# Kernel optimization log

Hardware: AMD Instinct MI355X
Metric: run time of the kernel (lower is better)

## Reference

```python
import jax, jax.numpy as jnp
import numpy as np

NUM_HEADS = 12
HEAD_DIM = 64
LOGIT_SCALE_MAX = 4.605170185988092  # log(1/0.01), open_clip default
EPS = 1e-12  # F.normalize eps


def setup_inputs() -> dict:
    key = jax.random.key(0)
    ks = jax.random.split(key, 8)
    N, L, C = 2, 2048, 768
    return {
        "x": jax.random.normal(ks[0], (N, L, C), dtype=jnp.float32),
        "in_proj_w": jax.random.normal(ks[1], (3 * C, C), dtype=jnp.float32) * 0.02,
        "in_proj_b": jax.random.normal(ks[2], (3 * C,), dtype=jnp.float32) * 0.02,
        "logit_scale": jax.random.normal(ks[3], (NUM_HEADS, 1, 1), dtype=jnp.float32),
        "learned_scale": jnp.ones((NUM_HEADS,), dtype=jnp.float32),
        "out_proj_w": jax.random.normal(ks[4], (C, C), dtype=jnp.float32) * 0.02,
        "out_proj_b": jax.random.normal(ks[5], (C,), dtype=jnp.float32) * 0.02,
        "attn_mask": jnp.zeros((L, L), dtype=jnp.float32),
    }


def _l2norm(t):
    # F.normalize(dim=-1): x / max(||x||, eps)
    n = jnp.linalg.norm(t, axis=-1, keepdims=True)
    return t / jnp.maximum(n, EPS)


def reference(x, in_proj_w, in_proj_b, logit_scale, learned_scale,
              out_proj_w, out_proj_b, attn_mask):
    N, L, C = x.shape
    H, D = NUM_HEADS, HEAD_DIM
    # packed QKV projection: [N, L, 3C]
    qkv = jnp.einsum("nlc,fc->nlf", x, in_proj_w) + in_proj_b
    q, k, v = jnp.split(qkv, 3, axis=-1)
    # [N, L, C] -> [N, H, L, D]
    to_heads = lambda t: t.reshape(N, L, H, D).transpose(0, 2, 1, 3)
    q, k, v = to_heads(q), to_heads(k), to_heads(v)
    # cosine attention with clamped exp logit scale per head
    attn = jnp.einsum("nhld,nhmd->nhlm", _l2norm(q), _l2norm(k))
    ls = jnp.exp(jnp.minimum(logit_scale, LOGIT_SCALE_MAX))  # [H,1,1]
    attn = attn * ls[None]  # broadcast over [N,H,L,L]
    attn = attn + attn_mask  # additive mask [L,L]
    attn = jax.nn.softmax(attn, axis=-1)
    out = jnp.einsum("nhlm,nhmd->nhld", attn, v)
    # learned per-head output scale
    out = out * learned_scale[None, :, None, None]
    # [N,H,L,D] -> [N,L,C]
    out = out.transpose(0, 2, 1, 3).reshape(N, L, C)
    out = jnp.einsum("nlc,fc->nlf", out, out_proj_w) + out_proj_b
    return out
```

## Files before the change

kernel.cpp:

```cpp
#include <hip/hip_runtime.h>
#include <math.h>

#define NB   2
#define SEQ  2048
#define CH   768
#define NH   12
#define HD   64
#define F3   2304
#define LSMAX 4.605170185988092f
#define LOG2E 1.4426950408889634f

typedef _Float16 f16;
typedef __attribute__((ext_vector_type(8))) _Float16 f16x8;
typedef __attribute__((ext_vector_type(4))) _Float16 f16x4;
typedef __attribute__((ext_vector_type(2))) _Float16 f16x2;
typedef __attribute__((ext_vector_type(4))) float f32x4;

typedef __attribute__((address_space(3))) void lds_void;
typedef __attribute__((address_space(1))) const void gbl_cvoid;

#define QSZ   3145728
#define OATT  (3 * QSZ)
#define XHOFF 12582912
#define W1OFF 15728640
#define W2OFF 17498112
#define FLAGO 18087936

#define KP   72
#define VP   136
#define PPIT 76
#define GP2  72

__global__ __launch_bounds__(256) void cvt_f16(const float* __restrict__ X,
                                               const float* __restrict__ W1,
                                               const float* __restrict__ W2,
                                               const float* __restrict__ M,
                                               f16* __restrict__ Xh,
                                               f16* __restrict__ W1h,
                                               f16* __restrict__ W2h,
                                               int* __restrict__ flag)
{
    int tid = blockIdx.x * 256 + threadIdx.x;
    if (blockIdx.y == 3) {
        if (tid < 1048576) {
            float4 v = ((const float4*)M)[tid];
            bool nz = (v.x != 0.f) || (v.y != 0.f) || (v.z != 0.f) || (v.w != 0.f);
            if (__any(nz) && (threadIdx.x & 63) == 0) atomicOr(flag, 1);
        }
        return;
    }
    const float* src; f16* dst; int n4;
    switch (blockIdx.y) {
        case 0:  src = X;  dst = Xh;  n4 = 786432;  break;
        case 1:  src = W1; dst = W1h; n4 = 442368;  break;
        default: src = W2; dst = W2h; n4 = 147456;  break;
    }
    if (tid < n4) {
        float4 v = ((const float4*)src)[tid];
        f16x4 o = {(f16)v.x, (f16)v.y, (f16)v.z, (f16)v.w};
        ((f16x4*)dst)[tid] = o;
    }
}

__global__ __launch_bounds__(256, 4) void qkv_gemm(const f16* __restrict__ Xh,
                                                   const f16* __restrict__ Wh,
                                                   const float* __restrict__ bias,
                                                   const float* __restrict__ logit_scale,
                                                   f16* __restrict__ qkv16)
{
    __shared__ f16 As[2][128 * 32];
    __shared__ f16 Bs[2][128 * 32];
    const int t    = threadIdx.x;
    const int w    = t >> 6;
    const int lane = t & 63;
    const int quad = lane >> 4;
    const int sub  = lane & 15;
    const int wm   = w & 1, wn = w >> 1;
    const int f0   = blockIdx.x * 128;
    const int m0   = blockIdx.y * 128;

    const int s0 = t, s1 = 256 + t;
    const int r0 = s0 >> 2, cb0 = ((s0 & 3) ^ (r0 & 3)) * 8;
    const int r1 = s1 >> 2, cb1 = ((s1 & 3) ^ (r1 & 3)) * 8;
    const f16* ga0 = Xh + (size_t)(m0 + r0) * CH + cb0;
    const f16* ga1 = Xh + (size_t)(m0 + r1) * CH + cb1;
    const f16* gb0 = Wh + (size_t)(f0 + r0) * CH + cb0;
    const f16* gb1 = Wh + (size_t)(f0 + r1) * CH + cb1;

    f32x4 acc[4][4];
#pragma unroll
    for (int i = 0; i < 4; ++i)
#pragma unroll
        for (int j = 0; j < 4; ++j) acc[i][j] = (f32x4){0.f, 0.f, 0.f, 0.f};

    const int pch = (quad ^ (sub & 3)) * 8;

    __builtin_amdgcn_global_load_lds((gbl_cvoid*)(ga0), (lds_void*)&As[0][s0 * 8], 16, 0, 0);
    __builtin_amdgcn_global_load_lds((gbl_cvoid*)(ga1), (lds_void*)&As[0][s1 * 8], 16, 0, 0);
    __builtin_amdgcn_global_load_lds((gbl_cvoid*)(gb0), (lds_void*)&Bs[0][s0 * 8], 16, 0, 0);
    __builtin_amdgcn_global_load_lds((gbl_cvoid*)(gb1), (lds_void*)&Bs[0][s1 * 8], 16, 0, 0);
    __syncthreads();

    for (int k0 = 0; k0 < CH; k0 += 32) {
        const int cur = (k0 >> 5) & 1, nxt = cur ^ 1;
        if (k0 + 32 < CH) {
            __builtin_amdgcn_global_load_lds((gbl_cvoid*)(ga0 + k0 + 32), (lds_void*)&As[nxt][s0 * 8], 16, 0, 0);
            __builtin_amdgcn_global_load_lds((gbl_cvoid*)(ga1 + k0 + 32), (lds_void*)&As[nxt][s1 * 8], 16, 0, 0);
            __builtin_amdgcn_global_load_lds((gbl_cvoid*)(gb0 + k0 + 32), (lds_void*)&Bs[nxt][s0 * 8], 16, 0, 0);
            __builtin_amdgcn_global_load_lds((gbl_cvoid*)(gb1 + k0 + 32), (lds_void*)&Bs[nxt][s1 * 8], 16, 0, 0);
        }
        f16x8 af[4], bf[4];
#pragma unroll
        for (int i = 0; i < 4; ++i) {
            af[i] = *(const f16x8*)&As[cur][(wm * 64 + i * 16 + sub) * 32 + pch];
            bf[i] = *(const f16x8*)&Bs[cur][(wn * 64 + i * 16 + sub) * 32 + pch];
        }
#pragma unroll
        for (int i = 0; i < 4; ++i)
#pragma unroll
            for (int j = 0; j < 4; ++j)
                acc[i][j] = __builtin_amdgcn_mfma_f32_16x16x32_f16(af[i], bf[j], acc[i][j], 0, 0, 0);
        __syncthreads();
    }

    const int t3 = f0 / CH;
    const int h  = ((f0 + wn * 64) % CH) >> 6;
    f16* dst = qkv16 + (size_t)t3 * QSZ;
    float lsv = (t3 == 0) ? __expf(fminf(logit_scale[h], LSMAX)) * LOG2E : 1.0f;
    float bb[4];
#pragma unroll
    for (int j = 0; j < 4; ++j) bb[j] = bias[f0 + wn * 64 + j * 16 + sub];
#pragma unroll
    for (int i = 0; i < 4; ++i) {
#pragma unroll
        for (int r = 0; r < 4; ++r) {
            int m = m0 + wm * 64 + i * 16 + quad * 4 + r;
            int n = m >> 11, l = m & 2047;
            float v[4];
#pragma unroll
            for (int j = 0; j < 4; ++j) v[j] = acc[i][j][r] + bb[j];
            float scale = 1.0f;
            if (t3 < 2) {
                float ss = v[0] * v[0] + v[1] * v[1] + v[2] * v[2] + v[3] * v[3];
#pragma unroll
                for (int mk = 1; mk < 16; mk <<= 1) ss += __shfl_xor(ss, mk, 64);
                scale = 1.0f / fmaxf(sqrtf(ss), 1e-12f);
                if (t3 == 0) scale *= lsv;
            }
            f16* drow = dst + (((size_t)n * NH + h) * SEQ + l) * HD;
#pragma unroll
            for (int j = 0; j < 4; ++j)
                drow[j * 16 + sub] = (f16)(v[j] * scale);
        }
    }
}

__global__ __launch_bounds__(256, 3) void attn(const f16* __restrict__ Qh,
                                               const f16* __restrict__ Kh,
                                               const f16* __restrict__ Vh,
                                               const float* __restrict__ M32,
                                               const float* __restrict__ lscale,
                                               const int* __restrict__ flag,
                                               f16* __restrict__ Og)
{
    __shared__ f16 Ks[128 * KP];
    __shared__ f16 Vt[64 * VP];
    __shared__ f16 QP[64 * PPIT];

    const int t    = threadIdx.x;
    const int w    = t >> 6;
    const int lane = t & 63;
    const int quad = lane >> 4;
    const int sub  = lane & 15;
    const int qb   = blockIdx.x * 64;
    const int h    = blockIdx.y, n = blockIdx.z;
    const bool has_mask = (*flag) != 0;

    const f16* Qg = Qh + ((size_t)(n * NH + h) * SEQ + qb) * HD;
    const f16* Kg = Kh + (size_t)(n * NH + h) * SEQ * HD;
    const f16* Vg = Vh + (size_t)(n * NH + h) * SEQ * HD;
    const float* Mg = M32 + (size_t)(qb + w * 16 + quad * 4) * SEQ;

#pragma unroll
    for (int rep = 0; rep < 2; ++rep) {
        int id = rep * 256 + t;
        int row = id >> 3, c8 = id & 7;
        f16x8 v = *(const f16x8*)&Qg[row * 64 + c8 * 8];
        *(f16x4*)&QP[row * PPIT + c8 * 8 + 0] = (f16x4){v[0], v[1], v[2], v[3]};
        *(f16x4*)&QP[row * PPIT + c8 * 8 + 4] = (f16x4){v[4], v[5], v[6], v[7]};
    }

    const int krow = t >> 1;
    const int kcb  = (t & 1) * 32;
    f16x8 kr0, kr1, kr2, kr3, vr0, vr1, vr2, vr3;
    {
        const f16* kp = Kg + krow * 64 + kcb;
        kr0 = *(const f16x8*)(kp + 0);
        kr1 = *(const f16x8*)(kp + 8);
        kr2 = *(const f16x8*)(kp + 16);
        kr3 = *(const f16x8*)(kp + 24);
        const f16* vp = Vg + (2 * lane) * 64 + w * 16;
        vr0 = *(const f16x8*)(vp + 0);
        vr1 = *(const f16x8*)(vp + 8);
        vr2 = *(const f16x8*)(vp + 64);
        vr3 = *(const f16x8*)(vp + 72);
    }

    __syncthreads();
    f16x8 qf0, qf1;
    {
        f16x4 l0 = *(const f16x4*)&QP[(w * 16 + sub) * PPIT + quad * 8];
        f16x4 l1 = *(const f16x4*)&QP[(w * 16 + sub) * PPIT + quad * 8 + 4];
        f16x4 l2 = *(const f16x4*)&QP[(w * 16 + sub) * PPIT + 32 + quad * 8];
        f16x4 l3 = *(const f16x4*)&QP[(w * 16 + sub) * PPIT + 32 + quad * 8 + 4];
        qf0 = (f16x8){l0[0], l0[1], l0[2], l0[3], l1[0], l1[1], l1[2], l1[3]};
        qf1 = (f16x8){l2[0], l2[1], l2[2], l2[3], l3[0], l3[1], l3[2], l3[3]};
    }

    {
        f16* kd = &Ks[krow * KP + kcb];
        *(f16x8*)(kd + 0)  = kr0;
        *(f16x8*)(kd + 8)  = kr1;
        *(f16x8*)(kd + 16) = kr2;
        *(f16x8*)(kd + 24) = kr3;
#pragma unroll
        for (int j = 0; j < 8; ++j) {
            *(f16x2*)&Vt[(w * 16 + j) * VP + 2 * lane]     = (f16x2){vr0[j], vr2[j]};
            *(f16x2*)&Vt[(w * 16 + 8 + j) * VP + 2 * lane] = (f16x2){vr1[j], vr3[j]};
        }
    }
    __syncthreads();

    const f16x8 ones = {(f16)1.f, (f16)1.f, (f16)1.f, (f16)1.f,
                        (f16)1.f, (f16)1.f, (f16)1.f, (f16)1.f};
    f32x4 o[4];
    f32x4 l_acc = (f32x4){0.f, 0.f, 0.f, 0.f};
    float m_run[4];
#pragma unroll
    for (int dt = 0; dt < 4; ++dt) o[dt] = (f32x4){0.f, 0.f, 0.f, 0.f};
#pragma unroll
    for (int r = 0; r < 4; ++r) m_run[r] = -1e30f;

    const int NITER = SEQ / 128;
    for (int c = 0; c < NITER; ++c) {
        const int c0 = c * 128;
        if (c + 1 < NITER) {
            const f16* kp = Kg + (c0 + 128 + krow) * 64 + kcb;
            kr0 = *(const f16x8*)(kp + 0);
            kr1 = *(const f16x8*)(kp + 8);
            kr2 = *(const f16x8*)(kp + 16);
            kr3 = *(const f16x8*)(kp + 24);
            const f16* vp = Vg + (c0 + 128 + 2 * lane) * 64 + w * 16;
            vr0 = *(const f16x8*)(vp + 0);
            vr1 = *(const f16x8*)(vp + 8);
            vr2 = *(const f16x8*)(vp + 64);
            vr3 = *(const f16x8*)(vp + 72);
        }

        f32x4 s[8];
#pragma unroll
        for (int ct = 0; ct < 8; ++ct) {
            f16x8 kf0 = *(const f16x8*)&Ks[(ct * 16 + sub) * KP + quad * 8];
            f16x8 kf1 = *(const f16x8*)&Ks[(ct * 16 + sub) * KP + 32 + quad * 8];
            f32x4 a = (f32x4){0.f, 0.f, 0.f, 0.f};
            a = __builtin_amdgcn_mfma_f32_16x16x32_f16(qf0, kf0, a, 0, 0, 0);
            a = __builtin_amdgcn_mfma_f32_16x16x32_f16(qf1, kf1, a, 0, 0, 0);
            s[ct] = a;
        }
        if (has_mask) {
#pragma unroll
            for (int ct = 0; ct < 8; ++ct)
#pragma unroll
                for (int r = 0; r < 4; ++r)
                    s[ct][r] += LOG2E * Mg[(size_t)r * SEQ + c0 + ct * 16 + sub];
        }
        float mnew[4];
#pragma unroll
        for (int r = 0; r < 4; ++r) {
            float a01 = fmaxf(s[0][r], s[1][r]), a23 = fmaxf(s[2][r], s[3][r]);
            float a45 = fmaxf(s[4][r], s[5][r]), a67 = fmaxf(s[6][r], s[7][r]);
            mnew[r] = fmaxf(fmaxf(fmaxf(a01, a23), fmaxf(a45, a67)), m_run[r]);
        }
        {
            union { f16x2 h; int i; } p0, p1, v0, v1;
            p0.h = (f16x2){(f16)mnew[0], (f16)mnew[1]};
            p1.h = (f16x2){(f16)mnew[2], (f16)mnew[3]};
#pragma unroll
            for (int mk = 1; mk < 16; mk <<= 1) {
                v0.i = __shfl_xor(p0.i, mk, 64);
                v1.i = __shfl_xor(p1.i, mk, 64);
                p0.h = __builtin_elementwise_max(p0.h, v0.h);
                p1.h = __builtin_elementwise_max(p1.h, v1.h);
            }
            mnew[0] = (float)p0.h[0]; mnew[1] = (float)p0.h[1];
            mnew[2] = (float)p1.h[0]; mnew[3] = (float)p1.h[1];
        }
        float alpha[4];
#pragma unroll
        for (int r = 0; r < 4; ++r) {
            alpha[r] = exp2f(m_run[r] - mnew[r]);
            m_run[r] = mnew[r];
        }
#pragma unroll
        for (int dt = 0; dt < 4; ++dt)
#pragma unroll
            for (int r = 0; r < 4; ++r) o[dt][r] *= alpha[r];
#pragma unroll
        for (int r = 0; r < 4; ++r) l_acc[r] *= alpha[r];

#pragma unroll
        for (int hf = 0; hf < 2; ++hf) {
#pragma unroll
            for (int ct = 0; ct < 4; ++ct)
#pragma unroll
                for (int r = 0; r < 4; ++r) {
                    float p = exp2f(s[hf * 4 + ct][r] - mnew[r]);
                    QP[(w * 16 + quad * 4 + r) * PPIT + ct * 16 + sub] = (f16)p;
                }
            f16x4 p00 = *(const f16x4*)&QP[(w * 16 + sub) * PPIT + quad * 8];
            f16x4 p01 = *(const f16x4*)&QP[(w * 16 + sub) * PPIT + quad * 8 + 4];
            f16x4 p10 = *(const f16x4*)&QP[(w * 16 + sub) * PPIT + 32 + quad * 8];
            f16x4 p11 = *(const f16x4*)&QP[(w * 16 + sub) * PPIT + 32 + quad * 8 + 4];
            f16x8 pf0 = {p00[0], p00[1], p00[2], p00[3], p01[0], p01[1], p01[2], p01[3]};
            f16x8 pf1 = {p10[0], p10[1], p10[2], p10[3], p11[0], p11[1], p11[2], p11[3]};
            l_acc = __builtin_amdgcn_mfma_f32_16x16x32_f16(pf0, ones, l_acc, 0, 0, 0);
            l_acc = __builtin_amdgcn_mfma_f32_16x16x32_f16(pf1, ones, l_acc, 0, 0, 0);
#pragma unroll
            for (int dt = 0; dt < 4; ++dt) {
                f16x8 vf0 = *(const f16x8*)&Vt[(dt * 16 + sub) * VP + hf * 64 + quad * 8];
                f16x8 vf1 = *(const f16x8*)&Vt[(dt * 16 + sub) * VP + hf * 64 + 32 + quad * 8];
                o[dt] = __builtin_amdgcn_mfma_f32_16x16x32_f16(pf0, vf0, o[dt], 0, 0, 0);
                o[dt] = __builtin_amdgcn_mfma_f32_16x16x32_f16(pf1, vf1, o[dt], 0, 0, 0);
            }
        }

        if (c + 1 < NITER) {
            __syncthreads();
            f16* kd = &Ks[krow * KP + kcb];
            *(f16x8*)(kd + 0)  = kr0;
            *(f16x8*)(kd + 8)  = kr1;
            *(f16x8*)(kd + 16) = kr2;
            *(f16x8*)(kd + 24) = kr3;
#pragma unroll
            for (int j = 0; j < 8; ++j) {
                *(f16x2*)&Vt[(w * 16 + j) * VP + 2 * lane]     = (f16x2){vr0[j], vr2[j]};
                *(f16x2*)&Vt[(w * 16 + 8 + j) * VP + 2 * lane] = (f16x2){vr1[j], vr3[j]};
            }
            __syncthreads();
        }
    }
    float lsc = lscale[h];
#pragma unroll
    for (int r = 0; r < 4; ++r) {
        float inv = lsc / l_acc[r];
        int q = qb + w * 16 + quad * 4 + r;
#pragma unroll
        for (int dt = 0; dt < 4; ++dt)
            Og[((size_t)n * SEQ + q) * CH + h * 64 + dt * 16 + sub] =
                (f16)(o[dt][r] * inv);
    }
}

__global__ __launch_bounds__(256, 4) void out_gemm(const f16* __restrict__ A,
                                                   const f16* __restrict__ Wh,
                                                   const float* __restrict__ bias,
                                                   float* __restrict__ out)
{
    __shared__ f16 As[64 * GP2];
    __shared__ f16 Bs[64 * GP2];
    const int t    = threadIdx.x;
    const int w    = t >> 6;
    const int lane = t & 63;
    const int quad = lane >> 4;
    const int sub  = lane & 15;
    const int f0   = blockIdx.x * 64;
    const int m0   = blockIdx.y * 64;
    const int srow = t >> 2;
    const int sk   = (t & 3) * 16;

    const f16* ag = A + (size_t)(m0 + srow) * CH + sk;
    const f16* bg = Wh + (size_t)(f0 + srow) * CH + sk;
    f16x8 a0 = *(const f16x8*)(ag);
    f16x8 a1 = *(const f16x8*)(ag + 8);
    f16x8 b0 = *(const f16x8*)(bg);
    f16x8 b1 = *(const f16x8*)(bg + 8);

    f32x4 acc[4];
#pragma unroll
    for (int i = 0; i < 4; ++i) acc[i] = (f32x4){0.f, 0.f, 0.f, 0.f};

    for (int k0 = 0; k0 < CH; k0 += 64) {
        __syncthreads();
        *(f16x8*)&As[srow * GP2 + sk + 0] = a0;
        *(f16x8*)&As[srow * GP2 + sk + 8] = a1;
        *(f16x8*)&Bs[srow * GP2 + sk + 0] = b0;
        *(f16x8*)&Bs[srow * GP2 + sk + 8] = b1;
        __syncthreads();
        if (k0 + 64 < CH) {
            a0 = *(const f16x8*)(ag + k0 + 64);
            a1 = *(const f16x8*)(ag + k0 + 72);
            b0 = *(const f16x8*)(bg + k0 + 64);
            b1 = *(const f16x8*)(bg + k0 + 72);
        }
#pragma unroll
        for (int kk = 0; kk < 64; kk += 32) {
            f16x8 bf = *(const f16x8*)&Bs[(w * 16 + sub) * GP2 + kk + quad * 8];
#pragma unroll
            for (int i = 0; i < 4; ++i) {
                f16x8 af = *(const f16x8*)&As[(i * 16 + sub) * GP2 + kk + quad * 8];
                acc[i] = __builtin_amdgcn_mfma_f32_16x16x32_f16(af, bf, acc[i], 0, 0, 0);
            }
        }
    }
    float bb = bias[f0 + w * 16 + sub];
#pragma unroll
    for (int i = 0; i < 4; ++i)
#pragma unroll
        for (int r = 0; r < 4; ++r) {
            int m = m0 + i * 16 + quad * 4 + r;
            out[(size_t)m * CH + f0 + w * 16 + sub] = acc[i][r] + bb;
        }
}

extern "C" void kernel_launch(void* const* d_in, const int* in_sizes, int n_in,
                              void* d_out, int out_size, void* d_ws, size_t ws_size,
                              hipStream_t stream) {
    const float* x    = (const float*)d_in[0];
    const float* w1   = (const float*)d_in[1];
    const float* b1   = (const float*)d_in[2];
    const float* ls   = (const float*)d_in[3];
    const float* lrn  = (const float*)d_in[4];
    const float* w2   = (const float*)d_in[5];
    const float* b2   = (const float*)d_in[6];
    const float* msk  = (const float*)d_in[7];
    f16*   ws16 = (f16*)d_ws;
    int*   flag = (int*)(ws16 + FLAGO);
    float* out  = (float*)d_out;

    (void)hipMemsetAsync(flag, 0, 4, stream);
    hipLaunchKernelGGL(cvt_f16, dim3(4096, 4), dim3(256), 0, stream,
                       x, w1, w2, msk,
                       ws16 + XHOFF, ws16 + W1OFF, ws16 + W2OFF, flag);
    hipLaunchKernelGGL(qkv_gemm, dim3(F3 / 128, (NB * SEQ) / 128), dim3(256), 0, stream,
                       ws16 + XHOFF, ws16 + W1OFF, b1, ls, ws16);
    hipLaunchKernelGGL(attn, dim3(SEQ / 64, NH, NB), dim3(256), 0, stream,
                       ws16, ws16 + QSZ, ws16 + 2 * QSZ, msk, lrn, flag,
                       ws16 + OATT);
    hipLaunchKernelGGL(out_gemm, dim3(CH / 64, (NB * SEQ) / 64), dim3(256), 0, stream,
                       ws16 + OATT, ws16 + W2OFF, b2, out);
}
```

Before: 209.5 us.

## Rewrite attention with 32x32 MFMA, transposed V, and split-KV within block

The QKV GEMM epilogue now writes V transposed ([N,H,D,L]) so the attention kernel can load V fragments straight from global memory without an LDS transpose. The attention kernel drops LDS staging of K/V entirely. It computes S^T with 32x32x16 MFMAs so each lane owns one query row's probabilities in registers, which removes the LDS round trip for P and the cross-lane max shuffles. Each block splits the key range between two wave pairs and merges the partial softmax states through LDS at the end. The cost is that K/V tiles are no longer shared through LDS, so global and cache traffic per wave rises.

```diff
diff --git a/kernel.cpp b/kernel.cpp
--- a/kernel.cpp
+++ b/kernel.cpp
@@ -15,6 +15,7 @@
 typedef __attribute__((ext_vector_type(4))) _Float16 f16x4;
 typedef __attribute__((ext_vector_type(2))) _Float16 f16x2;
 typedef __attribute__((ext_vector_type(4))) float f32x4;
+typedef __attribute__((ext_vector_type(16))) float f32x16;
 
 typedef __attribute__((address_space(3))) void lds_void;
 typedef __attribute__((address_space(1))) const void gbl_cvoid;
@@ -26,9 +27,6 @@
 #define W2OFF 17498112
 #define FLAGO 18087936
 
-#define KP   72
-#define VP   136
-#define PPIT 76
 #define GP2  72
 
 __global__ __launch_bounds__(256) void cvt_f16(const float* __restrict__ X,
@@ -125,11 +123,30 @@
 
     const int t3 = f0 / CH;
     const int h  = ((f0 + wn * 64) % CH) >> 6;
+    float bb[4];
+#pragma unroll
+    for (int j = 0; j < 4; ++j) bb[j] = bias[f0 + wn * 64 + j * 16 + sub];
+
+    if (t3 == 2) {
+        f16* vdst = qkv16 + (size_t)2 * QSZ;
+#pragma unroll
+        for (int i = 0; i < 4; ++i) {
+            int mb = m0 + wm * 64 + i * 16 + quad * 4;
+            int nn = mb >> 11, l0 = mb & 2047;
+            f16* vrow = vdst + ((size_t)(nn * NH + h) * HD) * SEQ + l0;
+#pragma unroll
+            for (int j = 0; j < 4; ++j) {
+                f16x4 vv;
+#pragma unroll
+                for (int r = 0; r < 4; ++r) vv[r] = (f16)(acc[i][j][r] + bb[j]);
+                *(f16x4*)(vrow + (size_t)(j * 16 + sub) * SEQ) = vv;
+            }
+        }
+        return;
+    }
+
     f16* dst = qkv16 + (size_t)t3 * QSZ;
     float lsv = (t3 == 0) ? __expf(fminf(logit_scale[h], LSMAX)) * LOG2E : 1.0f;
-    float bb[4];
-#pragma unroll
-    for (int j = 0; j < 4; ++j) bb[j] = bias[f0 + wn * 64 + j * 16 + sub];
 #pragma unroll
     for (int i = 0; i < 4; ++i) {
 #pragma unroll
@@ -139,14 +156,11 @@
             float v[4];
 #pragma unroll
             for (int j = 0; j < 4; ++j) v[j] = acc[i][j][r] + bb[j];
-            float scale = 1.0f;
-            if (t3 < 2) {
-                float ss = v[0] * v[0] + v[1] * v[1] + v[2] * v[2] + v[3] * v[3];
-#pragma unroll
-                for (int mk = 1; mk < 16; mk <<= 1) ss += __shfl_xor(ss, mk, 64);
-                scale = 1.0f / fmaxf(sqrtf(ss), 1e-12f);
-                if (t3 == 0) scale *= lsv;
-            }
+            float ss = v[0] * v[0] + v[1] * v[1] + v[2] * v[2] + v[3] * v[3];
+#pragma unroll
+            for (int mk = 1; mk < 16; mk <<= 1) ss += __shfl_xor(ss, mk, 64);
+            float scale = 1.0f / fmaxf(sqrtf(ss), 1e-12f);
+            if (t3 == 0) scale *= lsv;
             f16* drow = dst + (((size_t)n * NH + h) * SEQ + l) * HD;
 #pragma unroll
             for (int j = 0; j < 4; ++j)
@@ -157,207 +171,156 @@
 
 __global__ __launch_bounds__(256, 3) void attn(const f16* __restrict__ Qh,
                                                const f16* __restrict__ Kh,
-                                               const f16* __restrict__ Vh,
+                                               const f16* __restrict__ Vt,
                                                const float* __restrict__ M32,
                                                const float* __restrict__ lscale,
                                                const int* __restrict__ flag,
                                                f16* __restrict__ Og)
 {
-    __shared__ f16 Ks[128 * KP];
-    __shared__ f16 Vt[64 * VP];
-    __shared__ f16 QP[64 * PPIT];
+    __shared__ float OS[2][32][68];
+    __shared__ float MS[2][32];
+    __shared__ float LS[2][32];
 
     const int t    = threadIdx.x;
     const int w    = t >> 6;
     const int lane = t & 63;
-    const int quad = lane >> 4;
-    const int sub  = lane & 15;
+    const int g    = w >> 1;
+    const int s    = w & 1;
+    const int r32  = lane & 31;
+    const int h2   = lane >> 5;
     const int qb   = blockIdx.x * 64;
-    const int h    = blockIdx.y, n = blockIdx.z;
+    const int hh   = blockIdx.y, n = blockIdx.z;
     const bool has_mask = (*flag) != 0;
 
-    const f16* Qg = Qh + ((size_t)(n * NH + h) * SEQ + qb) * HD;
-    const f16* Kg = Kh + (size_t)(n * NH + h) * SEQ * HD;
-    const f16* Vg = Vh + (size_t)(n * NH + h) * SEQ * HD;
-    const float* Mg = M32 + (size_t)(qb + w * 16 + quad * 4) * SEQ;
-
-#pragma unroll
-    for (int rep = 0; rep < 2; ++rep) {
-        int id = rep * 256 + t;
-        int row = id >> 3, c8 = id & 7;
-        f16x8 v = *(const f16x8*)&Qg[row * 64 + c8 * 8];
-        *(f16x4*)&QP[row * PPIT + c8 * 8 + 0] = (f16x4){v[0], v[1], v[2], v[3]};
-        *(f16x4*)&QP[row * PPIT + c8 * 8 + 4] = (f16x4){v[4], v[5], v[6], v[7]};
-    }
-
-    const int krow = t >> 1;
-    const int kcb  = (t & 1) * 32;
-    f16x8 kr0, kr1, kr2, kr3, vr0, vr1, vr2, vr3;
-    {
-        const f16* kp = Kg + krow * 64 + kcb;
-        kr0 = *(const f16x8*)(kp + 0);
-        kr1 = *(const f16x8*)(kp + 8);
-        kr2 = *(const f16x8*)(kp + 16);
-        kr3 = *(const f16x8*)(kp + 24);
-        const f16* vp = Vg + (2 * lane) * 64 + w * 16;
-        vr0 = *(const f16x8*)(vp + 0);
-        vr1 = *(const f16x8*)(vp + 8);
-        vr2 = *(const f16x8*)(vp + 64);
-        vr3 = *(const f16x8*)(vp + 72);
-    }
-
+    const int q = qb + g * 32 + r32;
+    const f16* Qg  = Qh + ((size_t)(n * NH + hh) * SEQ + q) * HD + 8 * h2;
+    const f16* Kl  = Kh + ((size_t)(n * NH + hh) * SEQ + s * 1024 + r32) * HD + 8 * h2;
+    const f16* Vb0 = Vt + ((size_t)(n * NH + hh) * HD + r32) * SEQ + s * 1024 + 4 * h2;
+    const f16* Vb1 = Vb0 + (size_t)32 * SEQ;
+    const float* Mg = M32 + (size_t)q * SEQ + s * 1024;
+
+    f16x8 qf0 = *(const f16x8*)(Qg + 0);
+    f16x8 qf1 = *(const f16x8*)(Qg + 16);
+    f16x8 qf2 = *(const f16x8*)(Qg + 32);
+    f16x8 qf3 = *(const f16x8*)(Qg + 48);
+
+    f16x8 kf0 = *(const f16x8*)(Kl + 0);
+    f16x8 kf1 = *(const f16x8*)(Kl + 16);
+    f16x8 kf2 = *(const f16x8*)(Kl + 32);
+    f16x8 kf3 = *(const f16x8*)(Kl + 48);
+
+    f32x16 o0 = {}, o1 = {};
+    float m_run = -1e30f, l_acc = 0.f;
+    const f16x2 one2 = {(f16)1.f, (f16)1.f};
+
+#pragma unroll 1
+    for (int c = 0; c < 32; ++c) {
+        const int k0 = c * 32;
+        f32x16 sA = {};
+        sA = __builtin_amdgcn_mfma_f32_32x32x16_f16(kf0, qf0, sA, 0, 0, 0);
+        sA = __builtin_amdgcn_mfma_f32_32x32x16_f16(kf1, qf1, sA, 0, 0, 0);
+        sA = __builtin_amdgcn_mfma_f32_32x32x16_f16(kf2, qf2, sA, 0, 0, 0);
+        sA = __builtin_amdgcn_mfma_f32_32x32x16_f16(kf3, qf3, sA, 0, 0, 0);
+        if (c + 1 < 32) {
+            const f16* kp = Kl + (size_t)(k0 + 32) * HD;
+            kf0 = *(const f16x8*)(kp + 0);
+            kf1 = *(const f16x8*)(kp + 16);
+            kf2 = *(const f16x8*)(kp + 32);
+            kf3 = *(const f16x8*)(kp + 48);
+        }
+        union V8 { f16x4 h[2]; f16x8 v; };
+        V8 va, vb, vc, vd;
+        va.h[0] = *(const f16x4*)(Vb0 + k0 + 0);
+        va.h[1] = *(const f16x4*)(Vb0 + k0 + 8);
+        vb.h[0] = *(const f16x4*)(Vb0 + k0 + 16);
+        vb.h[1] = *(const f16x4*)(Vb0 + k0 + 24);
+        vc.h[0] = *(const f16x4*)(Vb1 + k0 + 0);
+        vc.h[1] = *(const f16x4*)(Vb1 + k0 + 8);
+        vd.h[0] = *(const f16x4*)(Vb1 + k0 + 16);
+        vd.h[1] = *(const f16x4*)(Vb1 + k0 + 24);
+
+        if (has_mask) {
+#pragma unroll
+            for (int rr = 0; rr < 16; ++rr) {
+                int kk = k0 + (rr & 3) + 8 * (rr >> 2) + 4 * h2;
+                sA[rr] += LOG2E * Mg[kk];
+            }
+        }
+        float mloc = sA[0];
+#pragma unroll
+        for (int rr = 1; rr < 16; ++rr) mloc = fmaxf(mloc, sA[rr]);
+        float mfull = fmaxf(mloc, __shfl_xor(mloc, 32, 64));
+        float mnew = fmaxf(m_run, mfull);
+        float al = exp2f(m_run - mnew);
+        m_run = mnew;
+        l_acc *= al;
+#pragma unroll
+        for (int rr = 0; rr < 16; ++rr) { o0[rr] *= al; o1[rr] *= al; }
+
+        float p[16];
+#pragma unroll
+        for (int rr = 0; rr < 16; ++rr) p[rr] = exp2f(sA[rr] - m_run);
+        union U8 { int i[4]; f16x8 v; };
+#define PK(a, b) ({ f16x2 _t = {(f16)(a), (f16)(b)}; __builtin_bit_cast(int, _t); })
+        U8 u0, u1;
+        u0.i[0] = PK(p[0], p[1]);   u0.i[1] = PK(p[2], p[3]);
+        u0.i[2] = PK(p[4], p[5]);   u0.i[3] = PK(p[6], p[7]);
+        u1.i[0] = PK(p[8], p[9]);   u1.i[1] = PK(p[10], p[11]);
+        u1.i[2] = PK(p[12], p[13]); u1.i[3] = PK(p[14], p[15]);
+#undef PK
+        f16x8 pf0 = u0.v, pf1 = u1.v;
+
+        l_acc = __builtin_amdgcn_fdot2(__builtin_bit_cast(f16x2, u0.i[0]), one2, l_acc, false);
+        l_acc = __builtin_amdgcn_fdot2(__builtin_bit_cast(f16x2, u0.i[1]), one2, l_acc, false);
+        l_acc = __builtin_amdgcn_fdot2(__builtin_bit_cast(f16x2, u0.i[2]), one2, l_acc, false);
+        l_acc = __builtin_amdgcn_fdot2(__builtin_bit_cast(f16x2, u0.i[3]), one2, l_acc, false);
+        l_acc = __builtin_amdgcn_fdot2(__builtin_bit_cast(f16x2, u1.i[0]), one2, l_acc, false);
+        l_acc = __builtin_amdgcn_fdot2(__builtin_bit_cast(f16x2, u1.i[1]), one2, l_acc, false);
+        l_acc = __builtin_amdgcn_fdot2(__builtin_bit_cast(f16x2, u1.i[2]), one2, l_acc, false);
+        l_acc = __builtin_amdgcn_fdot2(__builtin_bit_cast(f16x2, u1.i[3]), one2, l_acc, false);
+
+        o0 = __builtin_amdgcn_mfma_f32_32x32x16_f16(va.v, pf0, o0, 0, 0, 0);
+        o0 = __builtin_amdgcn_mfma_f32_32x32x16_f16(vb.v, pf1, o0, 0, 0, 0);
+        o1 = __builtin_amdgcn_mfma_f32_32x32x16_f16(vc.v, pf0, o1, 0, 0, 0);
+        o1 = __builtin_amdgcn_mfma_f32_32x32x16_f16(vd.v, pf1, o1, 0, 0, 0);
+    }
+
+    float l_full = l_acc + __shfl_xor(l_acc, 32, 64);
+
+    if (s == 1) {
+        if (h2 == 0) { MS[g][r32] = m_run; LS[g][r32] = l_full; }
+#pragma unroll
+        for (int rq = 0; rq < 4; ++rq) {
+            int d0 = 8 * rq + 4 * h2;
+            *(f32x4*)&OS[g][r32][d0] =
+                (f32x4){o0[rq * 4 + 0], o0[rq * 4 + 1], o0[rq * 4 + 2], o0[rq * 4 + 3]};
+            *(f32x4*)&OS[g][r32][d0 + 32] =
+                (f32x4){o1[rq * 4 + 0], o1[rq * 4 + 1], o1[rq * 4 + 2], o1[rq * 4 + 3]};
+        }
+    }
     __syncthreads();
-    f16x8 qf0, qf1;
-    {
-        f16x4 l0 = *(const f16x4*)&QP[(w * 16 + sub) * PPIT + quad * 8];
-        f16x4 l1 = *(const f16x4*)&QP[(w * 16 + sub) * PPIT + quad * 8 + 4];
-        f16x4 l2 = *(const f16x4*)&QP[(w * 16 + sub) * PPIT + 32 + quad * 8];
-        f16x4 l3 = *(const f16x4*)&QP[(w * 16 + sub) * PPIT + 32 + quad * 8 + 4];
-        qf0 = (f16x8){l0[0], l0[1], l0[2], l0[3], l1[0], l1[1], l1[2], l1[3]};
-        qf1 = (f16x8){l2[0], l2[1], l2[2], l2[3], l3[0], l3[1], l3[2], l3[3]};
-    }
-
-    {
-        f16* kd = &Ks[krow * KP + kcb];
-        *(f16x8*)(kd + 0)  = kr0;
-        *(f16x8*)(kd + 8)  = kr1;
-        *(f16x8*)(kd + 16) = kr2;
-        *(f16x8*)(kd + 24) = kr3;
-#pragma unroll
-        for (int j = 0; j < 8; ++j) {
-            *(f16x2*)&Vt[(w * 16 + j) * VP + 2 * lane]     = (f16x2){vr0[j], vr2[j]};
-            *(f16x2*)&Vt[(w * 16 + 8 + j) * VP + 2 * lane] = (f16x2){vr1[j], vr3[j]};
-        }
-    }
-    __syncthreads();
-
-    const f16x8 ones = {(f16)1.f, (f16)1.f, (f16)1.f, (f16)1.f,
-                        (f16)1.f, (f16)1.f, (f16)1.f, (f16)1.f};
-    f32x4 o[4];
-    f32x4 l_acc = (f32x4){0.f, 0.f, 0.f, 0.f};
-    float m_run[4];
-#pragma unroll
-    for (int dt = 0; dt < 4; ++dt) o[dt] = (f32x4){0.f, 0.f, 0.f, 0.f};
-#pragma unroll
-    for (int r = 0; r < 4; ++r) m_run[r] = -1e30f;
-
-    const int NITER = SEQ / 128;
-    for (int c = 0; c < NITER; ++c) {
-        const int c0 = c * 128;
-        if (c + 1 < NITER) {
-            const f16* kp = Kg + (c0 + 128 + krow) * 64 + kcb;
-            kr0 = *(const f16x8*)(kp + 0);
-            kr1 = *(const f16x8*)(kp + 8);
-            kr2 = *(const f16x8*)(kp + 16);
-            kr3 = *(const f16x8*)(kp + 24);
-            const f16* vp = Vg + (c0 + 128 + 2 * lane) * 64 + w * 16;
-            vr0 = *(const f16x8*)(vp + 0);
-            vr1 = *(const f16x8*)(vp + 8);
-            vr2 = *(const f16x8*)(vp + 64);
-            vr3 = *(const f16x8*)(vp + 72);
-        }
-
-        f32x4 s[8];
-#pragma unroll
-        for (int ct = 0; ct < 8; ++ct) {
-            f16x8 kf0 = *(const f16x8*)&Ks[(ct * 16 + sub) * KP + quad * 8];
-            f16x8 kf1 = *(const f16x8*)&Ks[(ct * 16 + sub) * KP + 32 + quad * 8];
-            f32x4 a = (f32x4){0.f, 0.f, 0.f, 0.f};
-            a = __builtin_amdgcn_mfma_f32_16x16x32_f16(qf0, kf0, a, 0, 0, 0);
-            a = __builtin_amdgcn_mfma_f32_16x16x32_f16(qf1, kf1, a, 0, 0, 0);
-            s[ct] = a;
-        }
-        if (has_mask) {
-#pragma unroll
-            for (int ct = 0; ct < 8; ++ct)
-#pragma unroll
-                for (int r = 0; r < 4; ++r)
-                    s[ct][r] += LOG2E * Mg[(size_t)r * SEQ + c0 + ct * 16 + sub];
-        }
-        float mnew[4];
-#pragma unroll
-        for (int r = 0; r < 4; ++r) {
-            float a01 = fmaxf(s[0][r], s[1][r]), a23 = fmaxf(s[2][r], s[3][r]);
-            float a45 = fmaxf(s[4][r], s[5][r]), a67 = fmaxf(s[6][r], s[7][r]);
-            mnew[r] = fmaxf(fmaxf(fmaxf(a01, a23), fmaxf(a45, a67)), m_run[r]);
-        }
-        {
-            union { f16x2 h; int i; } p0, p1, v0, v1;
-            p0.h = (f16x2){(f16)mnew[0], (f16)mnew[1]};
-            p1.h = (f16x2){(f16)mnew[2], (f16)mnew[3]};
-#pragma unroll
-            for (int mk = 1; mk < 16; mk <<= 1) {
-                v0.i = __shfl_xor(p0.i, mk, 64);
-                v1.i = __shfl_xor(p1.i, mk, 64);
-                p0.h = __builtin_elementwise_max(p0.h, v0.h);
-                p1.h = __builtin_elementwise_max(p1.h, v1.h);
+    if (s == 0) {
+        float m_p = MS[g][r32], l_p = LS[g][r32];
+        float mm = fmaxf(m_run, m_p);
+        float a0 = exp2f(m_run - mm), a1 = exp2f(m_p - mm);
+        float l_tot = a0 * l_full + a1 * l_p;
+        float sc = lscale[hh] / l_tot;
+        float sa = a0 * sc, sb = a1 * sc;
+        f16* op = Og + ((size_t)n * SEQ + q) * CH + hh * 64;
+#pragma unroll
+        for (int rq = 0; rq < 4; ++rq) {
+            int d0 = 8 * rq + 4 * h2;
+            f32x4 p0 = *(const f32x4*)&OS[g][r32][d0];
+            f32x4 p1 = *(const f32x4*)&OS[g][r32][d0 + 32];
+            f16x4 ov0, ov1;
+#pragma unroll
+            for (int j = 0; j < 4; ++j) {
+                ov0[j] = (f16)(o0[rq * 4 + j] * sa + p0[j] * sb);
+                ov1[j] = (f16)(o1[rq * 4 + j] * sa + p1[j] * sb);
             }
-            mnew[0] = (float)p0.h[0]; mnew[1] = (float)p0.h[1];
-            mnew[2] = (float)p1.h[0]; mnew[3] = (float)p1.h[1];
-        }
-        float alpha[4];
-#pragma unroll
-        for (int r = 0; r < 4; ++r) {
-            alpha[r] = exp2f(m_run[r] - mnew[r]);
-            m_run[r] = mnew[r];
-        }
-#pragma unroll
-        for (int dt = 0; dt < 4; ++dt)
-#pragma unroll
-            for (int r = 0; r < 4; ++r) o[dt][r] *= alpha[r];
-#pragma unroll
-        for (int r = 0; r < 4; ++r) l_acc[r] *= alpha[r];
-
-#pragma unroll
-        for (int hf = 0; hf < 2; ++hf) {
-#pragma unroll
-            for (int ct = 0; ct < 4; ++ct)
-#pragma unroll
-                for (int r = 0; r < 4; ++r) {
-                    float p = exp2f(s[hf * 4 + ct][r] - mnew[r]);
-                    QP[(w * 16 + quad * 4 + r) * PPIT + ct * 16 + sub] = (f16)p;
-                }
-            f16x4 p00 = *(const f16x4*)&QP[(w * 16 + sub) * PPIT + quad * 8];
-            f16x4 p01 = *(const f16x4*)&QP[(w * 16 + sub) * PPIT + quad * 8 + 4];
-            f16x4 p10 = *(const f16x4*)&QP[(w * 16 + sub) * PPIT + 32 + quad * 8];
-            f16x4 p11 = *(const f16x4*)&QP[(w * 16 + sub) * PPIT + 32 + quad * 8 + 4];
-            f16x8 pf0 = {p00[0], p00[1], p00[2], p00[3], p01[0], p01[1], p01[2], p01[3]};
-            f16x8 pf1 = {p10[0], p10[1], p10[2], p10[3], p11[0], p11[1], p11[2], p11[3]};
-            l_acc = __builtin_amdgcn_mfma_f32_16x16x32_f16(pf0, ones, l_acc, 0, 0, 0);
-            l_acc = __builtin_amdgcn_mfma_f32_16x16x32_f16(pf1, ones, l_acc, 0, 0, 0);
-#pragma unroll
-            for (int dt = 0; dt < 4; ++dt) {
-                f16x8 vf0 = *(const f16x8*)&Vt[(dt * 16 + sub) * VP + hf * 64 + quad * 8];
-                f16x8 vf1 = *(const f16x8*)&Vt[(dt * 16 + sub) * VP + hf * 64 + 32 + quad * 8];
-                o[dt] = __builtin_amdgcn_mfma_f32_16x16x32_f16(pf0, vf0, o[dt], 0, 0, 0);
-                o[dt] = __builtin_amdgcn_mfma_f32_16x16x32_f16(pf1, vf1, o[dt], 0, 0, 0);
-            }
-        }
-
-        if (c + 1 < NITER) {
-            __syncthreads();
-            f16* kd = &Ks[krow * KP + kcb];
-            *(f16x8*)(kd + 0)  = kr0;
-            *(f16x8*)(kd + 8)  = kr1;
-            *(f16x8*)(kd + 16) = kr2;
-            *(f16x8*)(kd + 24) = kr3;
-#pragma unroll
-            for (int j = 0; j < 8; ++j) {
-                *(f16x2*)&Vt[(w * 16 + j) * VP + 2 * lane]     = (f16x2){vr0[j], vr2[j]};
-                *(f16x2*)&Vt[(w * 16 + 8 + j) * VP + 2 * lane] = (f16x2){vr1[j], vr3[j]};
-            }
-            __syncthreads();
-        }
-    }
-    float lsc = lscale[h];
-#pragma unroll
-    for (int r = 0; r < 4; ++r) {
-        float inv = lsc / l_acc[r];
-        int q = qb + w * 16 + quad * 4 + r;
-#pragma unroll
-        for (int dt = 0; dt < 4; ++dt)
-            Og[((size_t)n * SEQ + q) * CH + h * 64 + dt * 16 + sub] =
-                (f16)(o[dt][r] * inv);
+            *(f16x4*)(op + d0)      = ov0;
+            *(f16x4*)(op + 32 + d0) = ov1;
+        }
     }
 }
 
```

Result: slower. 273.8 us (+30.7%).
